# Performance work log

Hardware: AMD Instinct MI355X
Metric: run time of the kernel (lower is better)

Reference implementation:

```python
import jax, jax.numpy as jnp
import numpy as np

N_NODES = 50000
N_EDGES = 800000
IN_CH = 64
HID_CH = 64
OUT_CH = 64
NUM_GRAPHS = 256


def setup_inputs() -> dict:
    key = jax.random.key(0)
    ks = jax.random.split(key, 9)
    x = jax.random.normal(ks[0], (N_NODES, IN_CH), dtype=jnp.float32)
    edge_index = jax.random.randint(ks[1], (2, N_EDGES), 0, N_NODES, dtype=jnp.int64)
    batch = jnp.sort(jax.random.randint(ks[2], (N_NODES,), 0, NUM_GRAPHS, dtype=jnp.int64))
    def glorot(k, fan_in, fan_out):
        s = jnp.sqrt(6.0 / (fan_in + fan_out))
        return jax.random.uniform(k, (fan_in, fan_out), jnp.float32, -s, s)
    W1 = glorot(ks[3], IN_CH, HID_CH)
    b1 = jnp.zeros((HID_CH,), jnp.float32)
    W2 = glorot(ks[4], HID_CH, HID_CH)
    b2 = jnp.zeros((HID_CH,), jnp.float32)
    W3 = glorot(ks[5], HID_CH, OUT_CH)
    b3 = jnp.zeros((OUT_CH,), jnp.float32)
    return {"x": x, "edge_index": edge_index, "batch": batch,
            "W1": W1, "b1": b1, "W2": W2, "b2": b2, "W3": W3, "b3": b3}


def gcn_conv(x, src, dst, W, b):
    # PyG GCNConv: linear, add self-loops, symmetric deg normalization, scatter-add, bias
    n = x.shape[0]
    xw = x @ W                                   # [N, F_out]
    loops = jnp.arange(n, dtype=src.dtype)
    s = jnp.concatenate([src, loops])            # sources (with self loops)
    d = jnp.concatenate([dst, loops])            # targets (with self loops)
    ones = jnp.ones(d.shape, dtype=x.dtype)
    deg = jax.ops.segment_sum(ones, d, num_segments=n)
    dinv = jnp.where(deg > 0, jax.lax.rsqrt(deg), 0.0)
    norm = dinv[s] * dinv[d]                     # [E + N]
    msgs = norm[:, None] * xw[s]                 # gather + scale
    out = jax.ops.segment_sum(msgs, d, num_segments=n)
    return out + b


def reference(x, edge_index, batch, W1, b1, W2, b2, W3, b3):
    src, dst = edge_index[0], edge_index[1]
    h = jax.nn.relu(gcn_conv(x, src, dst, W1, b1))
    h = jax.nn.relu(gcn_conv(h, src, dst, W2, b2))
    h = gcn_conv(h, src, dst, W3, b3)
    # global_add_pool over graph ids
    pooled = jax.ops.segment_sum(h, batch, num_segments=NUM_GRAPHS)  # [G, OUT_CH]
    return pooled  # out_channels != 1, so no flatten
```

## Files before the change

kernel.cpp:

```cpp
#include <hip/hip_runtime.h>
#include <hip/hip_bf16.h>

#define N_NODES 50000
#define N_EDGES 800000
#define CH 64
#define N_GRAPHS 256
#define NBUCK 196
#define CHUNK 8192

__device__ __forceinline__ unsigned bf16_rne(float f) {
    unsigned u = __float_as_uint(f);
    return (u + 0x7fffu + ((u >> 16) & 1u)) >> 16;
}
__device__ __forceinline__ float4 ldtab(const unsigned short* __restrict__ tab, int s, int c4) {
    uint2 u = *(const uint2*)(tab + ((size_t)s << 6) + c4);
    float4 r;
    r.x = __uint_as_float(u.x << 16);
    r.y = __uint_as_float(u.x & 0xffff0000u);
    r.z = __uint_as_float(u.y << 16);
    r.w = __uint_as_float(u.y & 0xffff0000u);
    return r;
}

__global__ void zero_ghist(int* __restrict__ g) {
    if (threadIdx.x < NBUCK) g[threadIdx.x] = 0;
}

__global__ void edge_hist(const int* __restrict__ ei, int* __restrict__ ghist) {
    __shared__ int h[NBUCK];
    for (int i = threadIdx.x; i < NBUCK; i += 256) h[i] = 0;
    __syncthreads();
    int t = blockIdx.x * 256 + threadIdx.x;
    int stride = gridDim.x * 256 * 4;
    for (int e = t * 4; e < N_EDGES; e += stride) {
        int4 d = *(const int4*)&ei[N_EDGES + e];
        atomicAdd(&h[d.x >> 8], 1);
        atomicAdd(&h[d.y >> 8], 1);
        atomicAdd(&h[d.z >> 8], 1);
        atomicAdd(&h[d.w >> 8], 1);
    }
    __syncthreads();
    for (int i = threadIdx.x; i < NBUCK; i += 256)
        if (h[i]) atomicAdd(&ghist[i], h[i]);
}

__global__ void bucket_scan(const int* __restrict__ ghist, int* __restrict__ bstart,
                            int* __restrict__ gcur, float* __restrict__ poolz) {
    int i = blockIdx.x * 256 + threadIdx.x;
    if (i < N_GRAPHS * CH + N_GRAPHS) poolz[i] = 0.0f;
    if (blockIdx.x != 0) return;
    __shared__ int sc[256];
    int tid = threadIdx.x;
    int v = (tid < NBUCK) ? ghist[tid] : 0;
    sc[tid] = v;
    __syncthreads();
    for (int off = 1; off < 256; off <<= 1) {
        int t = (tid >= off) ? sc[tid - off] : 0;
        __syncthreads();
        sc[tid] += t;
        __syncthreads();
    }
    if (tid < NBUCK) {
        int ex = sc[tid] - v;
        bstart[tid] = ex;
        gcur[tid] = ex;
    }
    if (tid == 255) bstart[NBUCK] = sc[255];
}

__global__ __launch_bounds__(512) void bin_scatter(const int* __restrict__ ei,
                                                   int* __restrict__ gcur,
                                                   int2* __restrict__ ebuf) {
    __shared__ int hist[NBUCK];
    __shared__ int lofs[NBUCK];
    __shared__ int gbase[NBUCK];
    __shared__ int cur[NBUCK];
    __shared__ int sc[512];
    __shared__ int2 stage[CHUNK];
    int tid = threadIdx.x;
    for (int i = tid; i < NBUCK; i += 512) hist[i] = 0;
    __syncthreads();
    int e0 = blockIdx.x * CHUNK;
    int n = min(CHUNK, N_EDGES - e0);
    int src[16], dst[16];
#pragma unroll
    for (int k = 0; k < 16; ++k) {
        int idx = k * 512 + tid;
        if (idx < n) {
            int e = e0 + idx;
            src[k] = ei[e];
            dst[k] = ei[N_EDGES + e];
            atomicAdd(&hist[dst[k] >> 8], 1);
        } else dst[k] = -1;
    }
    __syncthreads();
    int v = (tid < NBUCK) ? hist[tid] : 0;
    sc[tid] = v;
    __syncthreads();
    for (int off = 1; off < 512; off <<= 1) {
        int t = (tid >= off) ? sc[tid - off] : 0;
        __syncthreads();
        sc[tid] += t;
        __syncthreads();
    }
    if (tid < NBUCK) {
        int ex = sc[tid] - v;
        lofs[tid] = ex;
        cur[tid] = ex;
        gbase[tid] = v ? atomicAdd(&gcur[tid], v) : 0;
    }
    __syncthreads();
#pragma unroll
    for (int k = 0; k < 16; ++k) {
        if (dst[k] >= 0) {
            int p = atomicAdd(&cur[dst[k] >> 8], 1);
            stage[p] = make_int2(src[k], dst[k]);
        }
    }
    __syncthreads();
    for (int i = tid; i < n; i += 512) {
        int2 p = stage[i];
        int b = p.y >> 8;
        ebuf[gbase[b] + (i - lofs[b])] = p;
    }
}

__global__ void csr_bucket(const int2* __restrict__ ebuf, const int* __restrict__ bstart,
                           int* __restrict__ deg, int* __restrict__ rowp,
                           float* __restrict__ dinv, int* __restrict__ col) {
    __shared__ int nd[256];
    __shared__ int cur[256];
    __shared__ int sc[256];
    int b = blockIdx.x;
    int tid = threadIdx.x;
    nd[tid] = 0;
    __syncthreads();
    int es = bstart[b], ee = bstart[b + 1];
    for (int e = es + tid; e < ee; e += 256)
        atomicAdd(&nd[ebuf[e].y & 255], 1);
    __syncthreads();
    int v = nd[tid];
    sc[tid] = v;
    __syncthreads();
    for (int off = 1; off < 256; off <<= 1) {
        int t = (tid >= off) ? sc[tid - off] : 0;
        __syncthreads();
        sc[tid] += t;
        __syncthreads();
    }
    int node = b * 256 + tid;
    int lstart = es + sc[tid] - v;
    if (node < N_NODES) {
        deg[node] = v;
        rowp[node] = lstart;
        dinv[node] = rsqrtf((float)v + 1.0f);
    }
    cur[tid] = lstart;
    __syncthreads();
    for (int e = es + tid; e < ee; e += 256) {
        int2 p = ebuf[e];
        int pos = atomicAdd(&cur[p.y & 255], 1);
        col[pos] = p.x;
    }
}

__global__ void gemm_reg(const float* __restrict__ in, const float* __restrict__ W,
                         unsigned short* __restrict__ out, int n) {
    __shared__ float WT[64 * 68];
    int tid = threadIdx.x;
    for (int i = tid; i < 64 * 64; i += 256) {
        int k = i >> 6, c = i & 63;
        WT[c * 68 + k] = W[i];
    }
    __syncthreads();
    int lane = tid & 63;
    int wv = __builtin_amdgcn_readfirstlane(tid >> 6);
    int row0 = blockIdx.x * 32 + wv * 8;
    if (row0 >= n) return;
    float acc[8] = {0.f, 0.f, 0.f, 0.f, 0.f, 0.f, 0.f, 0.f};
#pragma unroll 2
    for (int k = 0; k < 64; k += 4) {
        float4 w = *(const float4*)&WT[lane * 68 + k];
#pragma unroll
        for (int r = 0; r < 8; ++r) {
            float4 xv = *(const float4*)&in[(size_t)(row0 + r) * 64 + k];
            acc[r] = fmaf(xv.x, w.x, acc[r]);
            acc[r] = fmaf(xv.y, w.y, acc[r]);
            acc[r] = fmaf(xv.z, w.z, acc[r]);
            acc[r] = fmaf(xv.w, w.w, acc[r]);
        }
    }
#pragma unroll
    for (int r = 0; r < 8; ++r)
        out[(size_t)(row0 + r) * 64 + lane] = (unsigned short)bf16_rne(acc[r]);
}

template <int OUT_BF16>
__global__ void agg_v4(const int* __restrict__ rowp, const int* __restrict__ deg,
                       const int* __restrict__ col, const float* __restrict__ dinv,
                       const unsigned short* __restrict__ tab, const float* __restrict__ bias,
                       void* __restrict__ outv, int do_relu) {
    int wv = __builtin_amdgcn_readfirstlane(threadIdx.x >> 6);
    int node = blockIdx.x * 4 + wv;
    int lane = threadIdx.x & 63;
    int q = lane >> 4;
    int c4 = (lane & 15) << 2;
    float dd = dinv[node];
    int cnt = deg[node];
    int start = rowp[node];
    float4 acc = make_float4(0.f, 0.f, 0.f, 0.f);
    if (q == 0) {
        float4 xs = ldtab(tab, node, c4);
        float dd2 = dd * dd;
        acc.x = xs.x * dd2; acc.y = xs.y * dd2; acc.z = xs.z * dd2; acc.w = xs.w * dd2;
    }
    int j = 0;
    for (; j + 8 <= cnt; j += 8) {
        int sA = col[start + j + q];
        int sB = col[start + j + 4 + q];
        float nA = dinv[sA] * dd;
        float nB = dinv[sB] * dd;
        float4 xA = ldtab(tab, sA, c4);
        float4 xB = ldtab(tab, sB, c4);
        acc.x = fmaf(nA, xA.x, acc.x); acc.y = fmaf(nA, xA.y, acc.y);
        acc.z = fmaf(nA, xA.z, acc.z); acc.w = fmaf(nA, xA.w, acc.w);
        acc.x = fmaf(nB, xB.x, acc.x); acc.y = fmaf(nB, xB.y, acc.y);
        acc.z = fmaf(nB, xB.z, acc.z); acc.w = fmaf(nB, xB.w, acc.w);
    }
    for (; j < cnt; j += 4) {
        int jj = j + q;
        bool valid = jj < cnt;
        int s = col[start + (valid ? jj : 0)];
        float nv = valid ? dinv[s] * dd : 0.0f;
        float4 xv = ldtab(tab, s, c4);
        acc.x = fmaf(nv, xv.x, acc.x); acc.y = fmaf(nv, xv.y, acc.y);
        acc.z = fmaf(nv, xv.z, acc.z); acc.w = fmaf(nv, xv.w, acc.w);
    }
    acc.x += __shfl_xor(acc.x, 16); acc.y += __shfl_xor(acc.y, 16);
    acc.z += __shfl_xor(acc.z, 16); acc.w += __shfl_xor(acc.w, 16);
    acc.x += __shfl_xor(acc.x, 32); acc.y += __shfl_xor(acc.y, 32);
    acc.z += __shfl_xor(acc.z, 32); acc.w += __shfl_xor(acc.w, 32);
    if (q == 0) {
        if (bias) {
            float4 bv = *(const float4*)&bias[c4];
            acc.x += bv.x; acc.y += bv.y; acc.z += bv.z; acc.w += bv.w;
        }
        if (do_relu) {
            acc.x = fmaxf(acc.x, 0.f); acc.y = fmaxf(acc.y, 0.f);
            acc.z = fmaxf(acc.z, 0.f); acc.w = fmaxf(acc.w, 0.f);
        }
        if (OUT_BF16) {
            uint2 o;
            o.x = bf16_rne(acc.x) | (bf16_rne(acc.y) << 16);
            o.y = bf16_rne(acc.z) | (bf16_rne(acc.w) << 16);
            *(uint2*)&((unsigned short*)outv)[((size_t)node << 6) + c4] = o;
        } else {
            *(float4*)&((float*)outv)[((size_t)node << 6) + c4] = acc;
        }
    }
}

__global__ void pool_seg(const float* __restrict__ h, const int* __restrict__ batch,
                         float* __restrict__ pool, float* __restrict__ cntg) {
    int ch = threadIdx.x & 63;
    int grp = threadIdx.x >> 6;
    int base = (blockIdx.x * 4 + grp) * 16;
    float acc = 0.0f;
    int curg = -1, runlen = 0;
    for (int n = 0; n < 16; ++n) {
        int node = base + n;
        if (node >= N_NODES) break;
        int g = batch[node];
        float v = h[((size_t)node << 6) + ch];
        if (g != curg) {
            if (curg >= 0) {
                atomicAdd(&pool[curg * 64 + ch], acc);
                if (ch == 0) atomicAdd(&cntg[curg], (float)runlen);
            }
            curg = g; acc = v; runlen = 1;
        } else { acc += v; runlen++; }
    }
    if (curg >= 0) {
        atomicAdd(&pool[curg * 64 + ch], acc);
        if (ch == 0) atomicAdd(&cntg[curg], (float)runlen);
    }
}

__global__ void out_gemm(const float* __restrict__ P, const float* __restrict__ cntg,
                         const float* __restrict__ W, const float* __restrict__ b,
                         float* __restrict__ out) {
    __shared__ float Ws[64 * 64];
    int tid = threadIdx.x;
    for (int i = tid; i < 64 * 64; i += 256) Ws[i] = W[i];
    __syncthreads();
    int lane = tid & 63;
    int g = blockIdx.x * 4 + (tid >> 6);
    if (g >= N_GRAPHS) return;
    float pv = P[g * 64 + lane];
    float acc = 0.0f;
#pragma unroll
    for (int k = 0; k < 64; ++k)
        acc = fmaf(__shfl(pv, k, 64), Ws[k * 64 + lane], acc);
    out[g * 64 + lane] = acc + cntg[g] * b[lane];
}

extern "C" void kernel_launch(void* const* d_in, const int* in_sizes, int n_in,
                              void* d_out, int out_size, void* d_ws, size_t ws_size,
                              hipStream_t stream) {
    const float* x   = (const float*)d_in[0];
    const int* ei    = (const int*)d_in[1];
    const int* batch = (const int*)d_in[2];
    const float* W1  = (const float*)d_in[3];
    const float* b1  = (const float*)d_in[4];
    const float* W2  = (const float*)d_in[5];
    const float* b2  = (const float*)d_in[6];
    const float* W3  = (const float*)d_in[7];
    const float* b3  = (const float*)d_in[8];
    float* out = (float*)d_out;

    char* ws = (char*)d_ws;
    float* dinv  = (float*)(ws);
    int*   DEG   = (int*)(ws + 200192);
    int*   ROWP  = (int*)(ws + 400384);
    int*   COL   = (int*)(ws + 600576);
    float* XW    = (float*)(ws + 3801600);
    int2*  EBUF  = (int2*)(ws + 3801600);
    float* ACC   = (float*)(ws + 16601600);
    float* POOL  = (float*)(ws + 29401600);
    float* CNT   = (float*)(ws + 29467136);
    int*   GHIST = (int*)(ws + 29468160);
    int*   BST   = (int*)(ws + 29469184);
    int*   GCUR  = (int*)(ws + 29470208);

    const int WAVE_NODE_BLK = N_NODES / 4;
    const int GEMM_BLK = (N_NODES + 31) / 32;
    const int SCAT_BLK = (N_EDGES + CHUNK - 1) / CHUNK;

    zero_ghist<<<1, 256, 0, stream>>>(GHIST);
    edge_hist<<<128, 256, 0, stream>>>(ei, GHIST);
    bucket_scan<<<65, 256, 0, stream>>>(GHIST, BST, GCUR, POOL);
    bin_scatter<<<SCAT_BLK, 512, 0, stream>>>(ei, GCUR, EBUF);
    csr_bucket<<<NBUCK, 256, 0, stream>>>(EBUF, BST, DEG, ROWP, dinv, COL);

    gemm_reg<<<GEMM_BLK, 256, 0, stream>>>(x, W1, (unsigned short*)XW, N_NODES);
    agg_v4<0><<<WAVE_NODE_BLK, 256, 0, stream>>>(ROWP, DEG, COL, dinv,
        (const unsigned short*)XW, b1, ACC, 1);

    gemm_reg<<<GEMM_BLK, 256, 0, stream>>>(ACC, W2, (unsigned short*)XW, N_NODES);
    agg_v4<1><<<WAVE_NODE_BLK, 256, 0, stream>>>(ROWP, DEG, COL, dinv,
        (const unsigned short*)XW, b2, ACC, 1);

    agg_v4<0><<<WAVE_NODE_BLK, 256, 0, stream>>>(ROWP, DEG, COL, dinv,
        (const unsigned short*)ACC, nullptr, XW, 0);
    pool_seg<<<(N_NODES + 63) / 64, 256, 0, stream>>>(XW, batch, POOL, CNT);
    out_gemm<<<N_GRAPHS / 4, 256, 0, stream>>>(POOL, CNT, W3, b3, out);
}
```

Before: 251.7 us.

## Cache per-edge norms across layers, drop atomic histogram, halve scatter chunk

The first aggregation now writes the per-edge normalisation factor (dinv[src]*dinv[dst]) into a CSR-aligned array, and the later two aggregations read it sequentially instead of doing a random dinv gather per edge. The global histogram no longer uses atomics and a zeroing kernel: each histogram block writes its own partial row, and the scan kernel sums the rows. The bin_scatter chunk is halved, which doubles the block count and shrinks per-block shared staging. The cost is extra norm writes in layer 1, a serial 98-row sum in the scan, and a larger workspace.

```diff
diff --git a/kernel.cpp b/kernel.cpp
--- a/kernel.cpp
+++ b/kernel.cpp
@@ -6,7 +6,8 @@
 #define CH 64
 #define N_GRAPHS 256
 #define NBUCK 196
-#define CHUNK 8192
+#define CHUNK 4096
+#define NHIST 98
 
 __device__ __forceinline__ unsigned bf16_rne(float f) {
     unsigned u = __float_as_uint(f);
@@ -22,16 +23,12 @@
     return r;
 }
 
-__global__ void zero_ghist(int* __restrict__ g) {
-    if (threadIdx.x < NBUCK) g[threadIdx.x] = 0;
-}
-
-__global__ void edge_hist(const int* __restrict__ ei, int* __restrict__ ghist) {
+__global__ void edge_hist(const int* __restrict__ ei, int* __restrict__ hpart) {
     __shared__ int h[NBUCK];
     for (int i = threadIdx.x; i < NBUCK; i += 256) h[i] = 0;
     __syncthreads();
     int t = blockIdx.x * 256 + threadIdx.x;
-    int stride = gridDim.x * 256 * 4;
+    int stride = NHIST * 256 * 4;
     for (int e = t * 4; e < N_EDGES; e += stride) {
         int4 d = *(const int4*)&ei[N_EDGES + e];
         atomicAdd(&h[d.x >> 8], 1);
@@ -41,17 +38,19 @@
     }
     __syncthreads();
     for (int i = threadIdx.x; i < NBUCK; i += 256)
-        if (h[i]) atomicAdd(&ghist[i], h[i]);
-}
-
-__global__ void bucket_scan(const int* __restrict__ ghist, int* __restrict__ bstart,
+        hpart[blockIdx.x * NBUCK + i] = h[i];
+}
+
+__global__ void bucket_scan(const int* __restrict__ hpart, int* __restrict__ bstart,
                             int* __restrict__ gcur, float* __restrict__ poolz) {
     int i = blockIdx.x * 256 + threadIdx.x;
     if (i < N_GRAPHS * CH + N_GRAPHS) poolz[i] = 0.0f;
     if (blockIdx.x != 0) return;
     __shared__ int sc[256];
     int tid = threadIdx.x;
-    int v = (tid < NBUCK) ? ghist[tid] : 0;
+    int v = 0;
+    if (tid < NBUCK)
+        for (int r = 0; r < NHIST; ++r) v += hpart[r * NBUCK + tid];
     sc[tid] = v;
     __syncthreads();
     for (int off = 1; off < 256; off <<= 1) {
@@ -82,9 +81,9 @@
     __syncthreads();
     int e0 = blockIdx.x * CHUNK;
     int n = min(CHUNK, N_EDGES - e0);
-    int src[16], dst[16];
-#pragma unroll
-    for (int k = 0; k < 16; ++k) {
+    int src[8], dst[8];
+#pragma unroll
+    for (int k = 0; k < 8; ++k) {
         int idx = k * 512 + tid;
         if (idx < n) {
             int e = e0 + idx;
@@ -111,7 +110,7 @@
     }
     __syncthreads();
 #pragma unroll
-    for (int k = 0; k < 16; ++k) {
+    for (int k = 0; k < 8; ++k) {
         if (dst[k] >= 0) {
             int p = atomicAdd(&cur[dst[k] >> 8], 1);
             stage[p] = make_int2(src[k], dst[k]);
@@ -195,9 +194,10 @@
         out[(size_t)(row0 + r) * 64 + lane] = (unsigned short)bf16_rne(acc[r]);
 }
 
-template <int OUT_BF16>
+template <int OUT_BF16, int USE_NRM, int WRITE_NRM>
 __global__ void agg_v4(const int* __restrict__ rowp, const int* __restrict__ deg,
                        const int* __restrict__ col, const float* __restrict__ dinv,
+                       float* nrm,
                        const unsigned short* __restrict__ tab, const float* __restrict__ bias,
                        void* __restrict__ outv, int do_relu) {
     int wv = __builtin_amdgcn_readfirstlane(threadIdx.x >> 6);
@@ -218,10 +218,20 @@
     for (; j + 8 <= cnt; j += 8) {
         int sA = col[start + j + q];
         int sB = col[start + j + 4 + q];
-        float nA = dinv[sA] * dd;
-        float nB = dinv[sB] * dd;
+        float nA, nB;
+        if (USE_NRM) {
+            nA = nrm[start + j + q];
+            nB = nrm[start + j + 4 + q];
+        } else {
+            nA = dinv[sA] * dd;
+            nB = dinv[sB] * dd;
+        }
         float4 xA = ldtab(tab, sA, c4);
         float4 xB = ldtab(tab, sB, c4);
+        if (WRITE_NRM && (lane & 15) == 0) {
+            nrm[start + j + q] = nA;
+            nrm[start + j + 4 + q] = nB;
+        }
         acc.x = fmaf(nA, xA.x, acc.x); acc.y = fmaf(nA, xA.y, acc.y);
         acc.z = fmaf(nA, xA.z, acc.z); acc.w = fmaf(nA, xA.w, acc.w);
         acc.x = fmaf(nB, xB.x, acc.x); acc.y = fmaf(nB, xB.y, acc.y);
@@ -231,7 +241,13 @@
         int jj = j + q;
         bool valid = jj < cnt;
         int s = col[start + (valid ? jj : 0)];
-        float nv = valid ? dinv[s] * dd : 0.0f;
+        float nv;
+        if (USE_NRM) {
+            nv = valid ? nrm[start + jj] : 0.0f;
+        } else {
+            nv = valid ? dinv[s] * dd : 0.0f;
+        }
+        if (WRITE_NRM && valid && (lane & 15) == 0) nrm[start + jj] = nv;
         float4 xv = ldtab(tab, s, c4);
         acc.x = fmaf(nv, xv.x, acc.x); acc.y = fmaf(nv, xv.y, acc.y);
         acc.z = fmaf(nv, xv.z, acc.z); acc.w = fmaf(nv, xv.w, acc.w);
@@ -323,34 +339,34 @@
     int*   DEG   = (int*)(ws + 200192);
     int*   ROWP  = (int*)(ws + 400384);
     int*   COL   = (int*)(ws + 600576);
-    float* XW    = (float*)(ws + 3801600);
-    int2*  EBUF  = (int2*)(ws + 3801600);
-    float* ACC   = (float*)(ws + 16601600);
-    float* POOL  = (float*)(ws + 29401600);
-    float* CNT   = (float*)(ws + 29467136);
-    int*   GHIST = (int*)(ws + 29468160);
-    int*   BST   = (int*)(ws + 29469184);
-    int*   GCUR  = (int*)(ws + 29470208);
+    float* NRM   = (float*)(ws + 3800576);
+    int*   HPART = (int*)(ws + 7000576);
+    int*   BST   = (int*)(ws + 7077888);
+    int*   GCUR  = (int*)(ws + 7078912);
+    float* XW    = (float*)(ws + 7080960);
+    int2*  EBUF  = (int2*)(ws + 7080960);
+    float* ACC   = (float*)(ws + 19880960);
+    float* POOL  = (float*)(ws + 32680960);
+    float* CNT   = (float*)(ws + 32746496);
 
     const int WAVE_NODE_BLK = N_NODES / 4;
     const int GEMM_BLK = (N_NODES + 31) / 32;
     const int SCAT_BLK = (N_EDGES + CHUNK - 1) / CHUNK;
 
-    zero_ghist<<<1, 256, 0, stream>>>(GHIST);
-    edge_hist<<<128, 256, 0, stream>>>(ei, GHIST);
-    bucket_scan<<<65, 256, 0, stream>>>(GHIST, BST, GCUR, POOL);
+    edge_hist<<<NHIST, 256, 0, stream>>>(ei, HPART);
+    bucket_scan<<<65, 256, 0, stream>>>(HPART, BST, GCUR, POOL);
     bin_scatter<<<SCAT_BLK, 512, 0, stream>>>(ei, GCUR, EBUF);
     csr_bucket<<<NBUCK, 256, 0, stream>>>(EBUF, BST, DEG, ROWP, dinv, COL);
 
     gemm_reg<<<GEMM_BLK, 256, 0, stream>>>(x, W1, (unsigned short*)XW, N_NODES);
-    agg_v4<0><<<WAVE_NODE_BLK, 256, 0, stream>>>(ROWP, DEG, COL, dinv,
+    agg_v4<0, 0, 1><<<WAVE_NODE_BLK, 256, 0, stream>>>(ROWP, DEG, COL, dinv, NRM,
         (const unsigned short*)XW, b1, ACC, 1);
 
     gemm_reg<<<GEMM_BLK, 256, 0, stream>>>(ACC, W2, (unsigned short*)XW, N_NODES);
-    agg_v4<1><<<WAVE_NODE_BLK, 256, 0, stream>>>(ROWP, DEG, COL, dinv,
+    agg_v4<1, 1, 0><<<WAVE_NODE_BLK, 256, 0, stream>>>(ROWP, DEG, COL, dinv, NRM,
         (const unsigned short*)XW, b2, ACC, 1);
 
-    agg_v4<0><<<WAVE_NODE_BLK, 256, 0, stream>>>(ROWP, DEG, COL, dinv,
+    agg_v4<0, 1, 0><<<WAVE_NODE_BLK, 256, 0, stream>>>(ROWP, DEG, COL, dinv, NRM,
         (const unsigned short*)ACC, nullptr, XW, 0);
     pool_seg<<<(N_NODES + 63) / 64, 256, 0, stream>>>(XW, batch, POOL, CNT);
     out_gemm<<<N_GRAPHS / 4, 256, 0, stream>>>(POOL, CNT, W3, b3, out);
```

Result: faster. 241.6 us (-4.0%).
